# Kernel tuning notes

Measured on AMD Instinct MI355X. Metric: run time of the kernel, lower is better.

## Reference

```python
import jax, jax.numpy as jnp
import numpy as np

BATCH, H, NFAM = 32768, 1024, 10


def setup_inputs() -> dict:
    key = jax.random.key(0)
    k1, k2, k3, k4 = jax.random.split(key, 4)
    scale1 = 1.0 / np.sqrt(2 * H)
    scale2 = 1.0 / np.sqrt(H)
    return {
        "features": jax.random.normal(k1, (BATCH, H), dtype=jnp.float32),
        "prototypes": jax.random.normal(k2, (NFAM, H), dtype=jnp.float32),
        "W1": jax.random.normal(k3, (2 * H, H), dtype=jnp.float32) * scale1,
        "b1": jnp.zeros((H,), dtype=jnp.float32),
        "W2": jax.random.normal(k4, (H, H), dtype=jnp.float32) * scale2,
        "b2": jnp.zeros((H,), dtype=jnp.float32),
    }


def reference(features, prototypes, W1, b1, W2, b2):
    # Squared euclidean distances via the norm trick (avoids [B, NFAM, H] blowup).
    # argmin over squared distances == argmin over cdist (sqrt is monotone).
    f2 = jnp.sum(features * features, axis=1, keepdims=True)        # [B, 1]
    p2 = jnp.sum(prototypes * prototypes, axis=1)                   # [NFAM]
    d2 = f2 + p2[None, :] - 2.0 * (features @ prototypes.T)         # [B, NFAM]
    nearest_idx = jnp.argmin(d2, axis=1)                            # [B]
    nearest_prototypes = prototypes[nearest_idx]                    # [B, H]
    combined = jnp.concatenate([features, nearest_prototypes], axis=1)  # [B, 2H]
    hidden = jax.nn.relu(combined @ W1 + b1)                        # [B, H]
    adapted = hidden @ W2 + b2                                      # [B, H]
    return adapted
```

## Files before the change

kernel.cpp:

```cpp
#include <hip/hip_runtime.h>
#include <stdint.h>
#include <stddef.h>

#define BATCH 32768
#define HDIM  1024
#define NFAM  10

typedef short bf16x8 __attribute__((ext_vector_type(8)));
typedef float f32x4  __attribute__((ext_vector_type(4)));

__device__ __forceinline__ unsigned short f2bf(float x) {
  unsigned int u = __builtin_bit_cast(unsigned int, x);
  u += 0x7fffu + ((u >> 16) & 1u);
  return (unsigned short)(u >> 16);
}

__device__ __forceinline__ void async_cp16(unsigned short* lds_dst, const unsigned short* g_src) {
  __builtin_amdgcn_global_load_lds(
      (const __attribute__((address_space(1))) unsigned int*)g_src,
      (__attribute__((address_space(3))) unsigned int*)lds_dst,
      16, 0, 0);
}

__global__ __launch_bounds__(256) void transpose_cast(
    const float* __restrict__ in, unsigned short* __restrict__ out, int R, int C) {
  __shared__ float tile[64][65];
  const int t = threadIdx.x;
  const int c = t & 63;
  const int r0 = t >> 6;
  const int rbase = blockIdx.y * 64, cbase = blockIdx.x * 64;
#pragma unroll
  for (int i = 0; i < 16; ++i) {
    int r = r0 + i * 4;
    tile[r][c] = in[(size_t)(rbase + r) * C + cbase + c];
  }
  __syncthreads();
#pragma unroll
  for (int i = 0; i < 16; ++i) {
    int r = r0 + i * 4;
    out[(size_t)(cbase + r) * R + rbase + c] = f2bf(tile[c][r]);
  }
}

__global__ __launch_bounds__(256) void proto_prep(
    const float* __restrict__ protos, float* __restrict__ p2) {
  __shared__ float red[4];
  const int j = blockIdx.x, t = threadIdx.x;
  float4 v = ((const float4*)(protos + (size_t)j * HDIM))[t];
  float s = v.x * v.x + v.y * v.y + v.z * v.z + v.w * v.w;
#pragma unroll
  for (int o = 32; o > 0; o >>= 1) s += __shfl_down(s, o);
  if ((t & 63) == 0) red[t >> 6] = s;
  __syncthreads();
  if (t == 0) p2[j] = red[0] + red[1] + red[2] + red[3];
}

__global__ __launch_bounds__(256) void proto_contrib(
    const float* __restrict__ protos, const float* __restrict__ W1,
    const float* __restrict__ b1, float* __restrict__ protoC) {
  __shared__ float red[4][64];
  const int j  = blockIdx.y;
  const int ln = threadIdx.x & 63;
  const int ks = threadIdx.x >> 6;
  const int n  = blockIdx.x * 64 + ln;
  const float* p = protos + (size_t)j * HDIM + ks * 256;
  const float* w = W1 + (size_t)(HDIM + ks * 256) * HDIM + n;
  float s = 0.f;
#pragma unroll 16
  for (int kk = 0; kk < 256; ++kk)
    s += p[kk] * w[(size_t)kk * HDIM];
  red[ks][ln] = s;
  __syncthreads();
  if (ks == 0)
    protoC[j * HDIM + n] = red[0][ln] + red[1][ln] + red[2][ln] + red[3][ln] + b1[n];
}

__global__ __launch_bounds__(256) void nearest_kernel(
    const float* __restrict__ feats, const float* __restrict__ protos,
    const float* __restrict__ p2, unsigned short* __restrict__ featsB,
    int* __restrict__ idx) {
  __shared__ float pl[NFAM * HDIM];
  const int t = threadIdx.x;
#pragma unroll
  for (int j = 0; j < NFAM; ++j)
    ((float4*)pl)[t + 256 * j] = ((const float4*)protos)[t + 256 * j];
  __syncthreads();

  const int wave = t >> 6, lane = t & 63;
  float P2[NFAM];
#pragma unroll
  for (int j = 0; j < NFAM; ++j) P2[j] = p2[j];

#pragma unroll
  for (int rr = 0; rr < 4; ++rr) {
    const int row = blockIdx.x * 16 + wave * 4 + rr;
    const float* f = feats + (size_t)row * HDIM;

    float dot[NFAM];
#pragma unroll
    for (int j = 0; j < NFAM; ++j) dot[j] = 0.f;
    float f2 = 0.f;

#pragma unroll
    for (int ch = 0; ch < 4; ++ch) {
      const int k4 = ch * 64 + lane;
      float4 v = ((const float4*)f)[k4];
      f2 += v.x * v.x + v.y * v.y + v.z * v.z + v.w * v.w;
#pragma unroll
      for (int j = 0; j < NFAM; ++j) {
        float4 p = ((const float4*)pl)[j * 256 + k4];
        dot[j] += v.x * p.x + v.y * p.y + v.z * p.z + v.w * p.w;
      }
      uint2 pk;
      pk.x = (unsigned)f2bf(v.x) | ((unsigned)f2bf(v.y) << 16);
      pk.y = (unsigned)f2bf(v.z) | ((unsigned)f2bf(v.w) << 16);
      *(uint2*)(featsB + (size_t)row * HDIM + k4 * 4) = pk;
    }

#pragma unroll
    for (int o = 32; o > 0; o >>= 1) {
      f2 += __shfl_down(f2, o);
#pragma unroll
      for (int j = 0; j < NFAM; ++j) dot[j] += __shfl_down(dot[j], o);
    }
    if (lane == 0) {
      int best = 0;
      float bd = f2 + P2[0] - 2.f * dot[0];
#pragma unroll
      for (int j = 1; j < NFAM; ++j) {
        float d = f2 + P2[j] - 2.f * dot[j];
        if (d < bd) { bd = d; best = j; }
      }
      idx[row] = best;
    }
  }
}

template <int EPI>
__global__ __launch_bounds__(512, 2) void gemm256(
    const unsigned short* __restrict__ A,
    const unsigned short* __restrict__ Bt,
    const int* __restrict__ idx,
    const float* __restrict__ protoC,
    const float* __restrict__ bias,
    unsigned short* __restrict__ outB,
    float* __restrict__ outF) {
  constexpr int K  = 1024;
  constexpr int NT = K / 64;
  __shared__ unsigned short ldsA[2 * 2 * 2 * 128 * 32];
  __shared__ unsigned short ldsB[2 * 2 * 2 * 128 * 32];

  const int t    = threadIdx.x;
  const int lane = t & 63;
  const int quad = lane >> 4;
  const int r16  = lane & 15;
  const int wid  = t >> 6;
  const int wm   = wid >> 2;
  const int wn   = wid & 3;

  const int b = blockIdx.x;
  const int rowBase = ((b >> 5) + (b & 7) * 16) * 256;
  const int colBase = ((b >> 3) & 3) * 256;

  const int sr = t >> 2;
  const int q  = (t & 3) ^ ((t >> 3) & 3);
  const unsigned short* pA = A  + (size_t)(rowBase + sr) * K + q * 8;
  const unsigned short* pB = Bt + (size_t)(colBase + sr) * K + q * 8;
  const int ldst = t * 8;

  const int pr = quad ^ ((r16 >> 1) & 3);

  f32x4 acc[2][2][4][2];
#pragma unroll
  for (int a0 = 0; a0 < 2; ++a0)
#pragma unroll
    for (int b0 = 0; b0 < 2; ++b0)
#pragma unroll
      for (int m0 = 0; m0 < 4; ++m0)
#pragma unroll
        for (int n0 = 0; n0 < 2; ++n0) acc[a0][b0][m0][n0] = (f32x4){0.f, 0.f, 0.f, 0.f};

#define STAGE_A(buf, h, kb)                                                        \
  {                                                                                \
    async_cp16(ldsA + (buf) * 16384 + (0 * 2 + (h)) * 4096 + ldst,                 \
               pA + (size_t)(h) * (128 * K) + (kb) + 0 * 32);                      \
    async_cp16(ldsA + (buf) * 16384 + (1 * 2 + (h)) * 4096 + ldst,                 \
               pA + (size_t)(h) * (128 * K) + (kb) + 1 * 32);                      \
  }
#define STAGE_B(buf, h, kb)                                                        \
  {                                                                                \
    async_cp16(ldsB + (buf) * 16384 + (0 * 2 + (h)) * 4096 + ldst,                 \
               pB + (size_t)(h) * (128 * K) + (kb) + 0 * 32);                      \
    async_cp16(ldsB + (buf) * 16384 + (1 * 2 + (h)) * 4096 + ldst,                 \
               pB + (size_t)(h) * (128 * K) + (kb) + 1 * 32);                      \
  }

  STAGE_A(0, 0, 0);
  STAGE_B(0, 0, 0);
  STAGE_A(0, 1, 0);
  STAGE_B(0, 1, 0);

  for (int kt = 0; kt < NT; ++kt) {
    const int p   = kt & 1;
    const int kbn = ((kt + 1) & (NT - 1)) * 64;
#pragma unroll
    for (int ph = 0; ph < 4; ++ph) {
      if (ph == 0)      STAGE_A(p ^ 1, 0, kbn)
      else if (ph == 1) STAGE_B(p ^ 1, 0, kbn)
      else if (ph == 2) STAGE_A(p ^ 1, 1, kbn)
      else              STAGE_B(p ^ 1, 1, kbn)

      if (ph == 3) asm volatile("s_waitcnt vmcnt(8)" ::: "memory");
      else         asm volatile("s_waitcnt vmcnt(6)" ::: "memory");
      asm volatile("s_barrier" ::: "memory");
      __builtin_amdgcn_sched_barrier(0);

      const int ah = ph & 1;
      const int bh = ph >> 1;

      bf16x8 av[2][4], bv[2][2];
#pragma unroll
      for (int s = 0; s < 2; ++s)
#pragma unroll
        for (int mi = 0; mi < 4; ++mi)
          av[s][mi] = *(const bf16x8*)(ldsA + p * 16384 + (s * 2 + ah) * 4096 +
                                       (wm * 64 + mi * 16 + r16) * 32 + pr * 8);
#pragma unroll
      for (int s = 0; s < 2; ++s)
#pragma unroll
        for (int ni = 0; ni < 2; ++ni)
          bv[s][ni] = *(const bf16x8*)(ldsB + p * 16384 + (s * 2 + bh) * 4096 +
                                       (wn * 32 + ni * 16 + r16) * 32 + pr * 8);

      __builtin_amdgcn_s_setprio(1);
#pragma unroll
      for (int s = 0; s < 2; ++s)
#pragma unroll
        for (int mi = 0; mi < 4; ++mi)
#pragma unroll
          for (int ni = 0; ni < 2; ++ni)
            acc[ah][bh][mi][ni] = __builtin_amdgcn_mfma_f32_16x16x32_bf16(
                av[s][mi], bv[s][ni], acc[ah][bh][mi][ni], 0, 0, 0);
      __builtin_amdgcn_s_setprio(0);
      __builtin_amdgcn_sched_barrier(0);
      asm volatile("s_barrier" ::: "memory");
    }
  }
#undef STAGE_A
#undef STAGE_B

#pragma unroll
  for (int ah = 0; ah < 2; ++ah) {
#pragma unroll
    for (int mi = 0; mi < 4; ++mi) {
      const int grow0 = rowBase + ah * 128 + wm * 64 + mi * 16 + quad * 4;
      int pid[4];
      if (EPI) {
#pragma unroll
        for (int r = 0; r < 4; ++r) pid[r] = idx[grow0 + r];
      }
#pragma unroll
      for (int bh = 0; bh < 2; ++bh) {
#pragma unroll
        for (int ni = 0; ni < 2; ++ni) {
          const int gcol = colBase + bh * 128 + wn * 32 + ni * 16 + r16;
          if (EPI) {
#pragma unroll
            for (int r = 0; r < 4; ++r) {
              float v = acc[ah][bh][mi][ni][r] + protoC[(size_t)pid[r] * HDIM + gcol];
              v = fmaxf(v, 0.0f);
              outB[(size_t)(grow0 + r) * 1024 + gcol] = f2bf(v);
            }
          } else {
            const float bv = bias[gcol];
#pragma unroll
            for (int r = 0; r < 4; ++r)
              outF[(size_t)(grow0 + r) * 1024 + gcol] = acc[ah][bh][mi][ni][r] + bv;
          }
        }
      }
    }
  }
}

extern "C" void kernel_launch(void* const* d_in, const int* in_sizes, int n_in,
                              void* d_out, int out_size, void* d_ws, size_t ws_size,
                              hipStream_t stream) {
  const float* feats  = (const float*)d_in[0];
  const float* protos = (const float*)d_in[1];
  const float* W1     = (const float*)d_in[2];
  const float* b1     = (const float*)d_in[3];
  const float* W2     = (const float*)d_in[4];
  const float* b2     = (const float*)d_in[5];
  float* out = (float*)d_out;

  unsigned short* featsB  = (unsigned short*)d_ws;
  unsigned short* hiddenB = featsB + (size_t)BATCH * HDIM;
  unsigned short* W1t     = hiddenB + (size_t)BATCH * HDIM;
  unsigned short* W2t     = W1t + (size_t)HDIM * HDIM;
  float* protoC = (float*)(W2t + (size_t)HDIM * HDIM);
  float* p2     = protoC + NFAM * HDIM;
  int* idx      = (int*)(p2 + NFAM + 2);

  transpose_cast<<<dim3(HDIM / 64, HDIM / 64), 256, 0, stream>>>(W1, W1t, HDIM, HDIM);
  transpose_cast<<<dim3(HDIM / 64, HDIM / 64), 256, 0, stream>>>(W2, W2t, HDIM, HDIM);
  proto_prep<<<NFAM, 256, 0, stream>>>(protos, p2);
  proto_contrib<<<dim3(HDIM / 64, NFAM), 256, 0, stream>>>(protos, W1, b1, protoC);
  nearest_kernel<<<BATCH / 16, 256, 0, stream>>>(feats, protos, p2, featsB, idx);
  gemm256<1><<<512, 512, 0, stream>>>(featsB, W1t, idx, protoC, nullptr, hiddenB, nullptr);
  gemm256<0><<<512, 512, 0, stream>>>(hiddenB, W2t, nullptr, nullptr, b2, nullptr, out);
}
```

Measured before the change: 479.4 us.

## Restructure GEMM main loop into 8-wave ping-pong with fragment reuse across quadrants

Reworks the K-loop schedule so the four 128x128 sub-quadrants are computed in the order (0,0),(0,1),(1,1),(1,0). This reuses A and B register fragments across consecutive phases instead of re-reading both from LDS every phase. Global-to-LDS prefetch now stages half-tiles two iterations ahead into the buffer half just consumed, with fewer vmcnt waits per iteration. The intent is to cut LDS read traffic and waits. The cost is more live registers, and the buffer-reuse ordering is fragile because of the write-after-read hazards on shared LDS halves.

```diff
diff --git a/kernel.cpp b/kernel.cpp
--- a/kernel.cpp
+++ b/kernel.cpp
@@ -194,60 +194,78 @@
     async_cp16(ldsB + (buf) * 16384 + (1 * 2 + (h)) * 4096 + ldst,                 \
                pB + (size_t)(h) * (128 * K) + (kb) + 1 * 32);                      \
   }
+#define READ_A(dst, p_, h)                                                          \
+  _Pragma("unroll")                                                                 \
+  for (int s = 0; s < 2; ++s)                                                       \
+    _Pragma("unroll")                                                               \
+    for (int mi = 0; mi < 4; ++mi)                                                  \
+      dst[s][mi] = *(const bf16x8*)(ldsA + (p_) * 16384 + (s * 2 + (h)) * 4096 +    \
+                                    (wm * 64 + mi * 16 + r16) * 32 + pr * 8);
+#define READ_B(dst, p_, h)                                                          \
+  _Pragma("unroll")                                                                 \
+  for (int s = 0; s < 2; ++s)                                                       \
+    _Pragma("unroll")                                                               \
+    for (int ni = 0; ni < 2; ++ni)                                                  \
+      dst[s][ni] = *(const bf16x8*)(ldsB + (p_) * 16384 + (s * 2 + (h)) * 4096 +    \
+                                    (wn * 32 + ni * 16 + r16) * 32 + pr * 8);
+#define MFMA_Q(ah, bh, bsrc)                                                        \
+  __builtin_amdgcn_s_setprio(1);                                                    \
+  _Pragma("unroll")                                                                 \
+  for (int s = 0; s < 2; ++s)                                                       \
+    _Pragma("unroll")                                                               \
+    for (int mi = 0; mi < 4; ++mi)                                                  \
+      _Pragma("unroll")                                                             \
+      for (int ni = 0; ni < 2; ++ni)                                                \
+        acc[ah][bh][mi][ni] = __builtin_amdgcn_mfma_f32_16x16x32_bf16(              \
+            av[s][mi], bsrc[s][ni], acc[ah][bh][mi][ni], 0, 0, 0);                  \
+  __builtin_amdgcn_s_setprio(0);
 
   STAGE_A(0, 0, 0);
+  STAGE_B(0, 1, 0);
+  STAGE_A(0, 1, 0);
   STAGE_B(0, 0, 0);
-  STAGE_A(0, 1, 0);
-  STAGE_B(0, 1, 0);
+  STAGE_A(1, 0, 64);
+  STAGE_B(1, 1, 64);
+  asm volatile("s_waitcnt vmcnt(4)" ::: "memory");
+  __builtin_amdgcn_s_barrier();
+
+  bf16x8 av[2][4], bvlo[2][2], bvhi[2][2];
 
   for (int kt = 0; kt < NT; ++kt) {
     const int p   = kt & 1;
-    const int kbn = ((kt + 1) & (NT - 1)) * 64;
-#pragma unroll
-    for (int ph = 0; ph < 4; ++ph) {
-      if (ph == 0)      STAGE_A(p ^ 1, 0, kbn)
-      else if (ph == 1) STAGE_B(p ^ 1, 0, kbn)
-      else if (ph == 2) STAGE_A(p ^ 1, 1, kbn)
-      else              STAGE_B(p ^ 1, 1, kbn)
-
-      if (ph == 3) asm volatile("s_waitcnt vmcnt(8)" ::: "memory");
-      else         asm volatile("s_waitcnt vmcnt(6)" ::: "memory");
-      asm volatile("s_barrier" ::: "memory");
-      __builtin_amdgcn_sched_barrier(0);
-
-      const int ah = ph & 1;
-      const int bh = ph >> 1;
-
-      bf16x8 av[2][4], bv[2][2];
-#pragma unroll
-      for (int s = 0; s < 2; ++s)
-#pragma unroll
-        for (int mi = 0; mi < 4; ++mi)
-          av[s][mi] = *(const bf16x8*)(ldsA + p * 16384 + (s * 2 + ah) * 4096 +
-                                       (wm * 64 + mi * 16 + r16) * 32 + pr * 8);
-#pragma unroll
-      for (int s = 0; s < 2; ++s)
-#pragma unroll
-        for (int ni = 0; ni < 2; ++ni)
-          bv[s][ni] = *(const bf16x8*)(ldsB + p * 16384 + (s * 2 + bh) * 4096 +
-                                       (wn * 32 + ni * 16 + r16) * 32 + pr * 8);
-
-      __builtin_amdgcn_s_setprio(1);
-#pragma unroll
-      for (int s = 0; s < 2; ++s)
-#pragma unroll
-        for (int mi = 0; mi < 4; ++mi)
-#pragma unroll
-          for (int ni = 0; ni < 2; ++ni)
-            acc[ah][bh][mi][ni] = __builtin_amdgcn_mfma_f32_16x16x32_bf16(
-                av[s][mi], bv[s][ni], acc[ah][bh][mi][ni], 0, 0, 0);
-      __builtin_amdgcn_s_setprio(0);
-      __builtin_amdgcn_sched_barrier(0);
-      asm volatile("s_barrier" ::: "memory");
-    }
+    const int kb1 = ((kt + 1) & (NT - 1)) * 64;
+    const int kb2 = ((kt + 2) & (NT - 1)) * 64;
+
+    READ_A(av, p, 0);
+    READ_B(bvlo, p, 0);
+    STAGE_A(p ^ 1, 1, kb1);
+    __builtin_amdgcn_s_barrier();
+    MFMA_Q(0, 0, bvlo);
+    __builtin_amdgcn_s_barrier();
+
+    READ_B(bvhi, p, 1);
+    STAGE_B(p ^ 1, 0, kb1);
+    __builtin_amdgcn_s_barrier();
+    MFMA_Q(0, 1, bvhi);
+    __builtin_amdgcn_s_barrier();
+
+    READ_A(av, p, 1);
+    STAGE_A(p, 0, kb2);
+    __builtin_amdgcn_s_barrier();
+    MFMA_Q(1, 1, bvhi);
+    __builtin_amdgcn_s_barrier();
+
+    STAGE_B(p, 1, kb2);
+    asm volatile("s_waitcnt vmcnt(4)" ::: "memory");
+    __builtin_amdgcn_s_barrier();
+    MFMA_Q(1, 0, bvlo);
+    __builtin_amdgcn_s_barrier();
   }
 #undef STAGE_A
 #undef STAGE_B
+#undef READ_A
+#undef READ_B
+#undef MFMA_Q
 
 #pragma unroll
   for (int ah = 0; ah < 2; ++ah) {
```

After: 413.2 us. 1.16x faster.
